# Performance work log

Hardware: AMD Instinct MI355X
Metric: run time of the kernel (lower is better)

## Reference

```python
import jax, jax.numpy as jnp
import numpy as np

N_NODES = 500_000
N_Q = 500_000
H = 8       # heads
MH = 8      # m // heads


def setup_inputs() -> dict:
    key = jax.random.key(0)
    ks = jax.random.split(key, 6)
    q_phi = jax.random.normal(ks[0], (N_Q, H, MH), dtype=jnp.float32)
    phi_k_pos = jax.random.normal(ks[1], (H, MH, N_NODES), dtype=jnp.float32)
    phi_k_neg = jax.random.normal(ks[2], (H, MH, N_NODES), dtype=jnp.float32)
    # degrees are nonnegative counts accumulated in build(); simulate with scaled uniforms
    deg_pos = jax.random.uniform(ks[3], (N_NODES, H), dtype=jnp.float32) * 32.0
    deg_neg = jax.random.uniform(ks[4], (N_NODES, H), dtype=jnp.float32) * 32.0
    k_indices = jax.random.randint(ks[5], (N_Q,), 0, N_NODES)
    return {
        "q_phi": q_phi,
        "phi_k_pos": phi_k_pos,
        "phi_k_neg": phi_k_neg,
        "deg_pos": deg_pos,
        "deg_neg": deg_neg,
        "k_indices": k_indices,
    }


def reference(q_phi, phi_k_pos, phi_k_neg, deg_pos, deg_neg, k_indices):
    # gather cached per-node random-feature sums: [h, mh, Nq] -> [Nq, h, mh]
    pk_pos = jnp.transpose(phi_k_pos[:, :, k_indices], (2, 0, 1))
    pk_neg = jnp.transpose(phi_k_neg[:, :, k_indices], (2, 0, 1))
    # per-head dot product over the feature chunk
    num_pos = jnp.sum(q_phi * pk_pos, axis=-1)  # [Nq, h]
    num_neg = jnp.sum(q_phi * pk_neg, axis=-1)  # [Nq, h]
    # degree-normalize with clamp_min(1)
    den_pos = jnp.maximum(deg_pos[k_indices], 1.0)  # [Nq, h]
    den_neg = jnp.maximum(deg_neg[k_indices], 1.0)
    return (num_pos / den_pos, num_neg / den_neg)
```

## Files before the change

### kernel.cpp

```cpp
#include <hip/hip_runtime.h>
#include <hip/hip_bf16.h>

constexpr int N_NODES = 500000;
constexpr int N_Q     = 500000;
constexpr int H       = 8;
constexpr int FEAT    = 64;
constexpr int NT      = (N_NODES + 63) / 64;


__global__ __launch_bounds__(256) void k_zero(int* __restrict__ cnt)
{
    const int i = blockIdx.x * 256 + threadIdx.x;
    if (i < NT) cnt[i] = 0;
}

__global__ __launch_bounds__(256) void k_hist(const int* __restrict__ k_idx,
                                              int* __restrict__ cnt)
{
    const int q = blockIdx.x * 256 + threadIdx.x;
    if (q < N_Q) atomicAdd(&cnt[k_idx[q] >> 6], 1);
}

__global__ __launch_bounds__(1024) void k_scan(const int* __restrict__ cnt,
                                               int* __restrict__ ofs,
                                               int* __restrict__ cursor)
{
    __shared__ int lds[1024];
    __shared__ int running;
    const int t = threadIdx.x;
    if (t == 0) running = 0;
    __syncthreads();
    for (int base = 0; base < NT; base += 1024) {
        const int i = base + t;
        const int v = (i < NT) ? cnt[i] : 0;
        lds[t] = v;
        __syncthreads();
        for (int off = 1; off < 1024; off <<= 1) {
            const int x = (t >= off) ? lds[t - off] : 0;
            __syncthreads();
            lds[t] += x;
            __syncthreads();
        }
        const int excl = lds[t] - v + running;
        if (i < NT) { ofs[i] = excl; cursor[i] = excl; }
        const int total = lds[1023];
        __syncthreads();
        if (t == 0) running += total;
        __syncthreads();
    }
}

__global__ __launch_bounds__(256) void k_scatter(const int* __restrict__ k_idx,
                                                 int* __restrict__ cursor,
                                                 int* __restrict__ perm)
{
    const int q = blockIdx.x * 256 + threadIdx.x;
    if (q < N_Q) {
        const int j = k_idx[q];
        const int p = atomicAdd(&cursor[j >> 6], 1);
        perm[p] = q | ((j & 63) << 19);
    }
}

__global__ __launch_bounds__(256) void k_main(
    const float* __restrict__ q_phi,
    const float* __restrict__ pk_pos,
    const float* __restrict__ pk_neg,
    const float* __restrict__ deg_pos,
    const float* __restrict__ deg_neg,
    const int*   __restrict__ perm,
    const int*   __restrict__ ofs,
    const int*   __restrict__ cnt,
    float*       __restrict__ out)
{
    __shared__ float lp[64 * 65];
    __shared__ float ln[64 * 65];

    const int t    = threadIdx.x;
    const int b    = blockIdx.x;
    const int n0   = b * 64;
    const int nrem = min(64, N_NODES - n0);

    {
        const int n4 = (t & 15) * 4;
        const int fb = t >> 4;
        for (int it = 0; it < 4; ++it) {
            const int f = fb + it * 16;
            const size_t off = (size_t)f * N_NODES + n0 + n4;
            float4 vp = make_float4(0.f, 0.f, 0.f, 0.f);
            float4 vn = make_float4(0.f, 0.f, 0.f, 0.f);
            if (n4 + 3 < nrem) {
                vp = *(const float4*)(pk_pos + off);
                vn = *(const float4*)(pk_neg + off);
            } else if (n4 < nrem) {
                vp.x = pk_pos[off]; vn.x = pk_neg[off];
                if (n4 + 1 < nrem) { vp.y = pk_pos[off + 1]; vn.y = pk_neg[off + 1]; }
                if (n4 + 2 < nrem) { vp.z = pk_pos[off + 2]; vn.z = pk_neg[off + 2]; }
            }
            float* wp = &lp[f * 65 + n4];
            float* wn = &ln[f * 65 + n4];
            wp[0] = vp.x; wp[1] = vp.y; wp[2] = vp.z; wp[3] = vp.w;
            wn[0] = vn.x; wn[1] = vn.y; wn[2] = vn.z; wn[3] = vn.w;
        }
    }
    __syncthreads();

    const int start = ofs[b];
    const int count = cnt[b];
    const int qi = t >> 3;
    const int h  = t & 7;

    for (int base = 0; base < count; base += 32) {
        const int k = base + qi;
        if (k < count) {
            const int v  = perm[start + k];
            const int q  = v & 0x7FFFF;
            const int jl = v >> 19;

            const float4* qp = (const float4*)(q_phi + (size_t)q * FEAT + h * 8);
            const float4 a0 = qp[0], a1 = qp[1];

            const float* rp = &lp[(h * 8) * 65 + jl];
            const float* rn = &ln[(h * 8) * 65 + jl];

            float sp = a0.x * rp[0]       + a0.y * rp[65]      + a0.z * rp[130]
                     + a0.w * rp[195]     + a1.x * rp[260]     + a1.y * rp[325]
                     + a1.z * rp[390]     + a1.w * rp[455];
            float sn = a0.x * rn[0]       + a0.y * rn[65]      + a0.z * rn[130]
                     + a0.w * rn[195]     + a1.x * rn[260]     + a1.y * rn[325]
                     + a1.z * rn[390]     + a1.w * rn[455];

            const int j = n0 + jl;
            const float dp = fmaxf(deg_pos[(size_t)j * H + h], 1.0f);
            const float dn = fmaxf(deg_neg[(size_t)j * H + h], 1.0f);

            const size_t o = (size_t)q * H + h;
            __builtin_nontemporal_store(sp / dp, &out[o]);
            __builtin_nontemporal_store(sn / dn, &out[(size_t)N_Q * H + o]);
        }
    }
}

__global__ __launch_bounds__(256, 4) void iskde_gather_kernel(
    const float* __restrict__ q_phi,
    const float* __restrict__ pk_pos,
    const float* __restrict__ pk_neg,
    const float* __restrict__ deg_pos,
    const float* __restrict__ deg_neg,
    const int*   __restrict__ k_idx,
    float*       __restrict__ out)
{
    const int wave_in_blk = threadIdx.x >> 6;
    const int lane        = threadIdx.x & 63;
    const int q           = blockIdx.x * 4 + wave_in_blk;
    if (q >= N_Q) return;

    const int j = k_idx[q];
    const float qv = q_phi[(size_t)q * FEAT + lane];
    const size_t col = (size_t)lane * (size_t)N_NODES + (size_t)j;
    const float pv = pk_pos[col];
    const float nv = pk_neg[col];

    float sp = qv * pv;
    float sn = qv * nv;
    sp += __shfl_xor(sp, 1, 64);
    sn += __shfl_xor(sn, 1, 64);
    sp += __shfl_xor(sp, 2, 64);
    sn += __shfl_xor(sn, 2, 64);
    sp += __shfl_xor(sp, 4, 64);
    sn += __shfl_xor(sn, 4, 64);

    if ((lane & 7) == 0) {
        const int h = lane >> 3;
        const float dp = fmaxf(deg_pos[(size_t)j * H + h], 1.0f);
        const float dn = fmaxf(deg_neg[(size_t)j * H + h], 1.0f);
        const size_t o = (size_t)q * H + h;
        out[o]                   = sp / dp;
        out[(size_t)N_Q * H + o] = sn / dn;
    }
}

extern "C" void kernel_launch(void* const* d_in, const int* in_sizes, int n_in,
                              void* d_out, int out_size, void* d_ws, size_t ws_size,
                              hipStream_t stream) {
    const float* q_phi   = (const float*)d_in[0];
    const float* pk_pos  = (const float*)d_in[1];
    const float* pk_neg  = (const float*)d_in[2];
    const float* deg_pos = (const float*)d_in[3];
    const float* deg_neg = (const float*)d_in[4];
    const int*   k_idx   = (const int*)d_in[5];
    float*       out     = (float*)d_out;

    const size_t need = ((size_t)N_Q + 3 * (size_t)NT) * sizeof(int);

    if (ws_size >= need) {
        int* perm   = (int*)d_ws;
        int* cnt    = perm + N_Q;
        int* ofs    = cnt + NT;
        int* cursor = ofs + NT;

        const int gq = (N_Q + 255) / 256;
        const int gt = (NT + 255) / 256;

        k_zero<<<gt, 256, 0, stream>>>(cnt);
        k_hist<<<gq, 256, 0, stream>>>(k_idx, cnt);
        k_scan<<<1, 1024, 0, stream>>>(cnt, ofs, cursor);
        k_scatter<<<gq, 256, 0, stream>>>(k_idx, cursor, perm);
        k_main<<<NT, 256, 0, stream>>>(q_phi, pk_pos, pk_neg,
                                       deg_pos, deg_neg, perm, ofs, cnt, out);
    } else {
        const int blocks = (N_Q + 3) / 4;
        iskde_gather_kernel<<<blocks, 256, 0, stream>>>(
            q_phi, pk_pos, pk_neg, deg_pos, deg_neg, k_idx, out);
    }
}
```

Baseline: 472.7 us.

## Replace per-tile LDS staging with flat sorted gather over bucketed queries

The main kernel no longer stages each 64-node tile of phi_k into shared memory and loops over the queries in that bucket. Instead the queries are still bucket-sorted by node tile, and one thread per (query, head) reads the eight feature values straight from global memory. Because neighbouring threads hit nearby nodes, the intent is to rely on cache locality while removing the load imbalance, the LDS fill and the sync barrier. The permutation entries become int2 (q, j), which doubles that buffer but drops the offsets array. The cost is strided, uncoalesced reads of the 64-row feature matrix, which depend on L2 reuse instead of an explicit tile load.

```diff
diff --git a/kernel.cpp b/kernel.cpp
--- a/kernel.cpp
+++ b/kernel.cpp
@@ -22,7 +22,6 @@
 }
 
 __global__ __launch_bounds__(1024) void k_scan(const int* __restrict__ cnt,
-                                               int* __restrict__ ofs,
                                                int* __restrict__ cursor)
 {
     __shared__ int lds[1024];
@@ -42,7 +41,7 @@
             __syncthreads();
         }
         const int excl = lds[t] - v + running;
-        if (i < NT) { ofs[i] = excl; cursor[i] = excl; }
+        if (i < NT) cursor[i] = excl;
         const int total = lds[1023];
         __syncthreads();
         if (t == 0) running += total;
@@ -52,93 +51,56 @@
 
 __global__ __launch_bounds__(256) void k_scatter(const int* __restrict__ k_idx,
                                                  int* __restrict__ cursor,
-                                                 int* __restrict__ perm)
+                                                 int2* __restrict__ perm)
 {
     const int q = blockIdx.x * 256 + threadIdx.x;
     if (q < N_Q) {
         const int j = k_idx[q];
         const int p = atomicAdd(&cursor[j >> 6], 1);
-        perm[p] = q | ((j & 63) << 19);
+        perm[p] = make_int2(q, j);
     }
 }
 
-__global__ __launch_bounds__(256) void k_main(
+__global__ __launch_bounds__(256) void k_gather_sorted(
     const float* __restrict__ q_phi,
     const float* __restrict__ pk_pos,
     const float* __restrict__ pk_neg,
     const float* __restrict__ deg_pos,
     const float* __restrict__ deg_neg,
-    const int*   __restrict__ perm,
-    const int*   __restrict__ ofs,
-    const int*   __restrict__ cnt,
+    const int2*  __restrict__ perm,
     float*       __restrict__ out)
 {
-    __shared__ float lp[64 * 65];
-    __shared__ float ln[64 * 65];
+    const int i = blockIdx.x * 256 + threadIdx.x;
+    const int p = i >> 3;
+    const int h = i & 7;
 
-    const int t    = threadIdx.x;
-    const int b    = blockIdx.x;
-    const int n0   = b * 64;
-    const int nrem = min(64, N_NODES - n0);
+    const int2 pj = perm[p];
+    const int q = pj.x;
+    const int j = pj.y;
 
-    {
-        const int n4 = (t & 15) * 4;
-        const int fb = t >> 4;
-        for (int it = 0; it < 4; ++it) {
-            const int f = fb + it * 16;
-            const size_t off = (size_t)f * N_NODES + n0 + n4;
-            float4 vp = make_float4(0.f, 0.f, 0.f, 0.f);
-            float4 vn = make_float4(0.f, 0.f, 0.f, 0.f);
-            if (n4 + 3 < nrem) {
-                vp = *(const float4*)(pk_pos + off);
-                vn = *(const float4*)(pk_neg + off);
-            } else if (n4 < nrem) {
-                vp.x = pk_pos[off]; vn.x = pk_neg[off];
-                if (n4 + 1 < nrem) { vp.y = pk_pos[off + 1]; vn.y = pk_neg[off + 1]; }
-                if (n4 + 2 < nrem) { vp.z = pk_pos[off + 2]; vn.z = pk_neg[off + 2]; }
-            }
-            float* wp = &lp[f * 65 + n4];
-            float* wn = &ln[f * 65 + n4];
-            wp[0] = vp.x; wp[1] = vp.y; wp[2] = vp.z; wp[3] = vp.w;
-            wn[0] = vn.x; wn[1] = vn.y; wn[2] = vn.z; wn[3] = vn.w;
-        }
-    }
-    __syncthreads();
+    const float4* qp = (const float4*)(q_phi + (size_t)q * FEAT + h * 8);
+    const float4 a0 = qp[0], a1 = qp[1];
 
-    const int start = ofs[b];
-    const int count = cnt[b];
-    const int qi = t >> 3;
-    const int h  = t & 7;
+    const float* bp = pk_pos + (size_t)(h * 8) * N_NODES + j;
+    const float* bn = pk_neg + (size_t)(h * 8) * N_NODES + j;
 
-    for (int base = 0; base < count; base += 32) {
-        const int k = base + qi;
-        if (k < count) {
-            const int v  = perm[start + k];
-            const int q  = v & 0x7FFFF;
-            const int jl = v >> 19;
+    float vp[8], vn[8];
+#pragma unroll
+    for (int f = 0; f < 8; ++f) vp[f] = bp[(size_t)f * N_NODES];
+#pragma unroll
+    for (int f = 0; f < 8; ++f) vn[f] = bn[(size_t)f * N_NODES];
 
-            const float4* qp = (const float4*)(q_phi + (size_t)q * FEAT + h * 8);
-            const float4 a0 = qp[0], a1 = qp[1];
+    const float sp = a0.x * vp[0] + a0.y * vp[1] + a0.z * vp[2] + a0.w * vp[3]
+                   + a1.x * vp[4] + a1.y * vp[5] + a1.z * vp[6] + a1.w * vp[7];
+    const float sn = a0.x * vn[0] + a0.y * vn[1] + a0.z * vn[2] + a0.w * vn[3]
+                   + a1.x * vn[4] + a1.y * vn[5] + a1.z * vn[6] + a1.w * vn[7];
 
-            const float* rp = &lp[(h * 8) * 65 + jl];
-            const float* rn = &ln[(h * 8) * 65 + jl];
+    const float dp = fmaxf(deg_pos[(size_t)j * H + h], 1.0f);
+    const float dn = fmaxf(deg_neg[(size_t)j * H + h], 1.0f);
 
-            float sp = a0.x * rp[0]       + a0.y * rp[65]      + a0.z * rp[130]
-                     + a0.w * rp[195]     + a1.x * rp[260]     + a1.y * rp[325]
-                     + a1.z * rp[390]     + a1.w * rp[455];
-            float sn = a0.x * rn[0]       + a0.y * rn[65]      + a0.z * rn[130]
-                     + a0.w * rn[195]     + a1.x * rn[260]     + a1.y * rn[325]
-                     + a1.z * rn[390]     + a1.w * rn[455];
-
-            const int j = n0 + jl;
-            const float dp = fmaxf(deg_pos[(size_t)j * H + h], 1.0f);
-            const float dn = fmaxf(deg_neg[(size_t)j * H + h], 1.0f);
-
-            const size_t o = (size_t)q * H + h;
-            __builtin_nontemporal_store(sp / dp, &out[o]);
-            __builtin_nontemporal_store(sn / dn, &out[(size_t)N_Q * H + o]);
-        }
-    }
+    const size_t o = (size_t)q * H + h;
+    __builtin_nontemporal_store(sp / dp, &out[o]);
+    __builtin_nontemporal_store(sn / dn, &out[(size_t)N_Q * H + o]);
 }
 
 __global__ __launch_bounds__(256, 4) void iskde_gather_kernel(
@@ -191,23 +153,24 @@
     const int*   k_idx   = (const int*)d_in[5];
     float*       out     = (float*)d_out;
 
-    const size_t need = ((size_t)N_Q + 3 * (size_t)NT) * sizeof(int);
+    const size_t need = (size_t)N_Q * sizeof(int2) + 2 * (size_t)NT * sizeof(int);
 
     if (ws_size >= need) {
-        int* perm   = (int*)d_ws;
-        int* cnt    = perm + N_Q;
-        int* ofs    = cnt + NT;
-        int* cursor = ofs + NT;
+        int2* perm   = (int2*)d_ws;
+        int*  cnt    = (int*)(perm + N_Q);
+        int*  cursor = cnt + NT;
 
         const int gq = (N_Q + 255) / 256;
         const int gt = (NT + 255) / 256;
 
         k_zero<<<gt, 256, 0, stream>>>(cnt);
         k_hist<<<gq, 256, 0, stream>>>(k_idx, cnt);
-        k_scan<<<1, 1024, 0, stream>>>(cnt, ofs, cursor);
+        k_scan<<<1, 1024, 0, stream>>>(cnt, cursor);
         k_scatter<<<gq, 256, 0, stream>>>(k_idx, cursor, perm);
-        k_main<<<NT, 256, 0, stream>>>(q_phi, pk_pos, pk_neg,
-                                       deg_pos, deg_neg, perm, ofs, cnt, out);
+
+        const int gm = (N_Q * H) / 256;
+        k_gather_sorted<<<gm, 256, 0, stream>>>(
+            q_phi, pk_pos, pk_neg, deg_pos, deg_neg, perm, out);
     } else {
         const int blocks = (N_Q + 3) / 4;
         iskde_gather_kernel<<<blocks, 256, 0, stream>>>(
```

New measurement: 502.2 us. 6.2% more time.
